# Performance work log

Hardware: AMD Instinct MI355X
Metric: run time of the kernel (lower is better)

The kernel has to match this reference:

```python
import jax, jax.numpy as jnp
import numpy as np

EPS = 1e-5  # BatchNorm eps (eval mode)
K_MAIN = 10
K_CORR = 8
LRELU = 0.2


def _knn_idx(x, k):
    # x: [B, c, n] -> [B, n, k] indices of k nearest neighbors (negative sq. distance top-k)
    inner = -2.0 * jnp.einsum('bcn,bcm->bnm', x, x)
    xx = jnp.sum(x * x, axis=1)                      # [B, n]
    pd = -xx[:, :, None] - inner - xx[:, None, :]    # [B, n, n]
    return jax.lax.top_k(pd, k)[1]


def _gather_neighbors(x, idx):
    # x: [B, c, n], idx: [B, n, k] -> [B, n, k, c]
    xt = jnp.transpose(x, (0, 2, 1))
    B = x.shape[0]
    return xt[jnp.arange(B)[:, None, None], idx]


def _graph_feature(x, k):
    # torch get_graph_feature: cat(neighbor - center, center) -> [B, 2c, n, k]
    idx = _knn_idx(x, k)
    neigh = _gather_neighbors(x, idx)                 # [B, n, k, c]
    xt = jnp.transpose(x, (0, 2, 1))                  # [B, n, c]
    center = jnp.broadcast_to(xt[:, :, None, :], neigh.shape)
    feat = jnp.concatenate([neigh - center, center], axis=-1)
    return jnp.transpose(feat, (0, 3, 1, 2))


def _branch(feat, w, g, b, m, v):
    # 1x1 Conv2d (no bias) + BatchNorm2d (eval) + LeakyReLU(0.2)
    y = jnp.einsum('oc,bcnk->bonk', w, feat)
    s = (g / jnp.sqrt(v + EPS))[None, :, None, None]
    y = (y - m[None, :, None, None]) * s + b[None, :, None, None]
    return jnp.where(y > 0, y, LRELU * y)


def _erase(x, masks, soft, w_e, b_e, g_e, be_e, m_e, v_e):
    # erase_feature: masked-softmax attention pooling + 1x1 conv_erase (conv+BN)
    soft = soft - (1.0 - masks) * 1e8
    sm = jax.nn.softmax(soft, axis=1)                 # [B, n]
    inp = x * masks[:, None, :]
    res = jnp.einsum('bcn,bn->bc', x, sm)             # [B, c]
    y = jnp.einsum('oc,bc->bo', w_e, res) + b_e
    y = (y - m_e) * (g_e / jnp.sqrt(v_e + EPS)) + be_e
    return inp + y[:, :, None]


def _corre_binar(x0_, x2, w_reduce):
    # x0_: [B, c] (detached query), x2: [B, c, n]
    B, c, n = x2.shape
    q = jnp.einsum('oc,bc->bo', w_reduce, x0_)        # conv_reduce (1x1, no bias)
    scale = 1.0 / jnp.sqrt(jnp.asarray(c, x2.dtype))
    f = jnp.einsum('bc,bcn->bn', q, x2) * scale       # [B, n]
    idx8 = _knn_idx(x2, K_CORR)                       # [B, n, 8]
    neigh = _gather_neighbors(x2, idx8)               # [B, n, 8, c]
    fk = jnp.einsum('bc,bnkc->bnk', q, neigh) * scale
    fk = f + jnp.sum(fk, axis=-1)                     # [B, n]
    index = jnp.argmax(fk, axis=1)                    # [B]
    ib = jnp.arange(B)
    masks = jnp.zeros((B, n), x2.dtype).at[ib, index].set(1.0)
    index_k = idx8[ib, index]                         # [B, 8] neighbors of argmax point
    masks = masks.at[ib[:, None], index_k].set(1.0)
    return 1.0 - masks, f


def _forward(x, w_reduce, w_erase, b_erase, g_erase, be_erase, m_erase, v_erase,
             w0, g0, b0, m0, v0, w1, g1, b1, m1, v1):
    b, t, c, n = x.shape
    B = b * t
    x1seq = jnp.concatenate([x[:, 1:], x[:, -1:]], axis=1).reshape(B, c, n)
    ones = jnp.ones((B, n), x.dtype)
    x0 = _erase(x.reshape(B, c, n), ones, ones,
                w_erase, b_erase, g_erase, be_erase, m_erase, v_erase)
    y0 = jnp.max(_branch(_graph_feature(x0, K_MAIN), w0, g0, b0, m0, v0), axis=-1)  # [B, O, n]
    x0_vec = jnp.max(y0, axis=-1)                                                    # [B, O]
    p0 = jnp.concatenate([jnp.max(y0, axis=-1), jnp.mean(y0, axis=-1)], axis=1)
    masks, soft = _corre_binar(jax.lax.stop_gradient(x0_vec), x1seq, w_reduce)
    x1e = _erase(x1seq, masks, soft,
                 w_erase, b_erase, g_erase, be_erase, m_erase, v_erase)
    y1 = jnp.max(_branch(_graph_feature(x1e, K_MAIN), w1, g1, b1, m1, v1), axis=-1)
    p1 = jnp.concatenate([jnp.max(y1, axis=-1), jnp.mean(y1, axis=-1)], axis=1)
    return p0 + p1                                                                   # [B, 2*O]


def setup_inputs() -> dict:
    key = jax.random.key(0)
    ks = jax.random.split(key, 20)
    b, t, c, n, out = 8, 12, 64, 512, 64
    sc = np.sqrt(2.0 / c).astype(np.float32)
    scb = np.sqrt(2.0 / out).astype(np.float32)
    f32 = jnp.float32
    inp = {
        'x': jax.random.normal(ks[0], (b, t, c, n), f32),
        'w_reduce': jax.random.normal(ks[1], (c, c), f32) * sc,
        'w_erase': jax.random.normal(ks[2], (c, c), f32) * sc,
        'b_erase': jax.random.normal(ks[3], (c,), f32) * 0.01,
        'g_erase': jax.random.uniform(ks[4], (c,), f32, 0.5, 1.5),
        'be_erase': jax.random.normal(ks[5], (c,), f32) * 0.1,
        'm_erase': jax.random.normal(ks[6], (c,), f32) * 0.1,
        'v_erase': jax.random.uniform(ks[7], (c,), f32, 0.5, 1.5),
        'w0': jax.random.normal(ks[8], (out, 2 * c), f32) * scb,
        'g0': jax.random.uniform(ks[9], (out,), f32, 0.5, 1.5),
        'b0': jax.random.normal(ks[10], (out,), f32) * 0.1,
        'm0': jax.random.normal(ks[11], (out,), f32) * 0.1,
        'v0': jax.random.uniform(ks[12], (out,), f32, 0.5, 1.5),
        'w1': jax.random.normal(ks[13], (out, 2 * c), f32) * scb,
        'g1': jax.random.uniform(ks[14], (out,), f32, 0.5, 1.5),
        'b1': jax.random.normal(ks[15], (out,), f32) * 0.1,
        'm1': jax.random.normal(ks[16], (out,), f32) * 0.1,
        'v1': jax.random.uniform(ks[17], (out,), f32, 0.5, 1.5),
    }
    return inp


def reference(x, w_reduce, w_erase, b_erase, g_erase, be_erase, m_erase, v_erase,
              w0, g0, b0, m0, v0, w1, g1, b1, m1, v1):
    return _forward(x, w_reduce, w_erase, b_erase, g_erase, be_erase, m_erase, v_erase,
                    w0, g0, b0, m0, v0, w1, g1, b1, m1, v1)
```

## Files before the change

kernel.cpp:

```cpp
#include <hip/hip_runtime.h>
#include <math.h>

#define EPS 1e-5f

typedef _Float16 half8 __attribute__((ext_vector_type(8)));
typedef float f32x4 __attribute__((ext_vector_type(4)));


__device__ __forceinline__ int src_row(int bq) {
    int b = bq / 12, t = bq - b * 12;
    int t2 = (t + 1 < 12) ? (t + 1) : 11;
    return b * 12 + t2;
}

__global__ __launch_bounds__(256) void prep_kernel(
    const float* __restrict__ X,
    _Float16* __restrict__ H, _Float16* __restrict__ L, float* __restrict__ xn,
    const float* __restrict__ w0, const float* __restrict__ w1,
    _Float16* __restrict__ wh0, _Float16* __restrict__ wl0,
    _Float16* __restrict__ wh1, _Float16* __restrict__ wl1,
    const float* __restrict__ w_e, const float* __restrict__ b_e,
    const float* __restrict__ g_e, const float* __restrict__ be_e,
    const float* __restrict__ m_e, const float* __restrict__ v_e,
    float* __restrict__ bias0)
{
    __shared__ float lds[64 * 65];
    __shared__ float xnp[4 * 64];
    __shared__ float part[256];
    __shared__ float res[64];
    __shared__ float sy[64];
    int raw = blockIdx.x;
    int tid = threadIdx.x;
    if (raw >= 768) {
        int bq = raw - 768;
        int c = tid >> 2, p = tid & 3;
        const float* xb = X + (size_t)bq * 32768 + c * 512 + p * 128;
        float acc = 0.f;
        for (int ii = 0; ii < 128; ii += 4) {
            float4 v = *(const float4*)(xb + ii);
            acc += v.x + v.y + v.z + v.w;
        }
        part[tid] = acc;
        __syncthreads();
        if (p == 0) res[c] = (part[tid] + part[tid+1] + part[tid+2] + part[tid+3]) * (1.f/512.f);
        __syncthreads();
        if (tid < 64) {
            float a = b_e[tid];
            for (int cc = 0; cc < 64; ++cc) a += w_e[tid*64+cc] * res[cc];
            float s = g_e[tid] / sqrtf(v_e[tid] + EPS);
            sy[tid] = (a - m_e[tid]) * s + be_e[tid];
        }
        __syncthreads();
        if (tid < 64) {
            float a = 0.f;
            for (int cc = 0; cc < 64; ++cc) a += w0[tid * 128 + 64 + cc] * sy[cc];
            bias0[bq * 64 + tid] = a;
        }
        return;
    }
    int bq = raw % 96;
    int ct = raw / 96;
    const float* Xb = X + (size_t)bq * 32768 + ct * 64;
    for (int p = 0; p < 16; ++p) {
        int t = p * 256 + tid;
        int c = t >> 6, col = t & 63;
        lds[c * 65 + col] = Xb[c * 512 + col];
    }
    __syncthreads();
    int col = tid & 63, g = tid >> 6;
    half8 hv[2], lv[2];
    float s = 0.f;
    #pragma unroll
    for (int k = 0; k < 16; ++k) {
        int c = g * 16 + k;
        float v = lds[c * 65 + col];
        _Float16 h = (_Float16)v;
        _Float16 lo = (_Float16)(v - (float)h);
        hv[k >> 3][k & 7] = h;
        lv[k >> 3][k & 7] = lo;
        s += v * v;
    }
    size_t obase = (size_t)bq * 32768 + ((size_t)(ct * 8 + 2 * g) * 64 + col) * 8;
    *(half8*)(H + obase) = hv[0];
    *(half8*)(H + obase + 512) = hv[1];
    *(half8*)(L + obase) = lv[0];
    *(half8*)(L + obase + 512) = lv[1];
    xnp[g * 64 + col] = s;
    __syncthreads();
    if (tid < 64)
        xn[bq * 512 + ct * 64 + tid] =
            xnp[tid] + xnp[64 + tid] + xnp[128 + tid] + xnp[192 + tid];
    if (raw < 2) {
        const float* W = raw ? w1 : w0;
        _Float16* WH = raw ? wh1 : wh0;
        _Float16* WL = raw ? wl1 : wl0;
        for (int t = tid; t < 8192; t += 256) {
            int o = t >> 6, c = t & 63;
            float v = (o < 64) ? W[o * 128 + c]
                               : (W[(o - 64) * 128 + 64 + c] - W[(o - 64) * 128 + c]);
            _Float16 h = (_Float16)v;
            WH[t] = h;
            WL[t] = (_Float16)(v - (float)h);
        }
    }
}

__global__ __launch_bounds__(256, 4) void knn_kernel(
    const _Float16* __restrict__ H, const _Float16* __restrict__ L,
    const float* __restrict__ xn,
    unsigned short* __restrict__ idx_out, unsigned short* __restrict__ key_out)
{
    __shared__ float4 jbuf[2048];
    int raw = blockIdx.x;
    int bq = raw % 96;
    int itile = raw / 96;
    int tid = threadIdx.x, w = tid >> 6, l = tid & 63;
    int lane16 = l & 15, quad = l >> 4;
    const size_t base = (size_t)bq * 32768;
    const _Float16* Hb = H + base;
    const _Float16* Lb = L + base;

    int irow = itile * 64 + w * 16 + lane16;
    size_t bo = ((size_t)(itile * 8 + quad) * 64 + (w * 16 + lane16)) * 8;
    half8 Bh0 = *(const half8*)(Hb + bo);
    half8 Bh1 = *(const half8*)(Hb + bo + 2048);
    half8 Bl0 = *(const half8*)(Lb + bo);
    half8 Bl1 = *(const half8*)(Lb + bo + 2048);

    unsigned kv[20];
    #pragma unroll
    for (int qq = 0; qq < 20; ++qq) kv[qq] = 0u;

    auto casu = [](unsigned& a, unsigned& b) {
        unsigned mn = a < b ? a : b;
        unsigned mx = a < b ? b : a;
        a = mn; b = mx;
    };

    const float* xnb = xn + bq * 512;
    float4* jbH = jbuf;
    float4* jbL = jbuf + 1024;
    {
        const float4* gh = (const float4*)(Hb);
        const float4* gl = (const float4*)(Lb);
        jbH[tid] = gh[tid]; jbH[256 + tid] = gh[256 + tid];
        jbL[tid] = gl[tid]; jbL[256 + tid] = gl[256 + tid];
    }
    __syncthreads();
    for (int jt = 0; jt < 8; ++jt) {
        int cur = jt & 1;
        float4 pa0, pa1, pb0, pb1;
        if (jt < 7) {
            const float4* gh = (const float4*)(Hb + (jt + 1) * 4096);
            const float4* gl = (const float4*)(Lb + (jt + 1) * 4096);
            pa0 = gh[tid]; pa1 = gh[256 + tid];
            pb0 = gl[tid]; pb1 = gl[256 + tid];
        }
        const _Float16* jH = (const _Float16*)(jbH + cur * 512);
        const _Float16* jL = (const _Float16*)(jbL + cur * 512);
        unsigned scb = (unsigned)((7 - jt) << 4);
        unsigned d[16];
        #pragma unroll
        for (int g = 0; g < 4; ++g) {
            int u = quad * 64 + g * 16 + lane16;
            half8 Ah0 = *(const half8*)(jH + (size_t)u * 8);
            half8 Ah1 = *(const half8*)(jH + (size_t)u * 8 + 2048);
            half8 Al0 = *(const half8*)(jL + (size_t)u * 8);
            half8 Al1 = *(const half8*)(jL + (size_t)u * 8 + 2048);
            f32x4 acc = {0.f, 0.f, 0.f, 0.f};
            acc = __builtin_amdgcn_mfma_f32_16x16x32_f16(Ah0, Bh0, acc, 0, 0, 0);
            acc = __builtin_amdgcn_mfma_f32_16x16x32_f16(Ah1, Bh1, acc, 0, 0, 0);
            acc = __builtin_amdgcn_mfma_f32_16x16x32_f16(Al0, Bh0, acc, 0, 0, 0);
            acc = __builtin_amdgcn_mfma_f32_16x16x32_f16(Al1, Bh1, acc, 0, 0, 0);
            acc = __builtin_amdgcn_mfma_f32_16x16x32_f16(Ah0, Bl0, acc, 0, 0, 0);
            acc = __builtin_amdgcn_mfma_f32_16x16x32_f16(Ah1, Bl1, acc, 0, 0, 0);
            int jb = jt * 64 + g * 16 + quad * 4;
            float4 xn4 = *(const float4*)&xnb[jb];
            #pragma unroll
            for (int r = 0; r < 4; ++r) {
                float xnr = (r == 0 ? xn4.x : r == 1 ? xn4.y : r == 2 ? xn4.z : xn4.w);
                float sc = fmaf(2.f, acc[r], -xnr);
                int bi = __float_as_int(sc);
                unsigned u2 = (unsigned)(bi ^ ((bi >> 31) | 0x80000000));
                int slot = g * 4 + r;
                d[slot] = (u2 & 0xFFFFFF80u) | (scb | (unsigned)(15 - slot));
            }
        }
        #pragma unroll
        for (int p = 1; p < 16; p <<= 1) {
            #pragma unroll
            for (int k = p; k >= 1; k >>= 1) {
                #pragma unroll
                for (int j = k & (p - 1); j + k < 16; j += 2 * k) {
                    #pragma unroll
                    for (int i = 0; i < k; ++i) {
                        if ((i + j + k < 16) &&
                            ((i + j) / (2 * p) == (i + j + k) / (2 * p)))
                            casu(d[i + j], d[i + j + k]);
                    }
                }
            }
        }
        #pragma unroll
        for (int i = 0; i < 16; ++i) {
            unsigned dv = d[15 - i];
            kv[i] = kv[i] > dv ? kv[i] : dv;
        }
        casu(kv[0],kv[16]); casu(kv[1],kv[17]); casu(kv[2],kv[18]); casu(kv[3],kv[19]);
        casu(kv[0],kv[8]);  casu(kv[1],kv[9]);  casu(kv[2],kv[10]); casu(kv[3],kv[11]);
        casu(kv[4],kv[12]); casu(kv[5],kv[13]); casu(kv[6],kv[14]); casu(kv[7],kv[15]);
        casu(kv[0],kv[4]);  casu(kv[1],kv[5]);  casu(kv[2],kv[6]);  casu(kv[3],kv[7]);
        casu(kv[8],kv[12]); casu(kv[9],kv[13]); casu(kv[10],kv[14]); casu(kv[11],kv[15]);
        casu(kv[0],kv[2]);  casu(kv[1],kv[3]);  casu(kv[4],kv[6]);  casu(kv[5],kv[7]);
        casu(kv[8],kv[10]); casu(kv[9],kv[11]); casu(kv[12],kv[14]); casu(kv[13],kv[15]);
        casu(kv[16],kv[18]); casu(kv[17],kv[19]);
        casu(kv[0],kv[1]);  casu(kv[2],kv[3]);  casu(kv[4],kv[5]);  casu(kv[6],kv[7]);
        casu(kv[8],kv[9]);  casu(kv[10],kv[11]); casu(kv[12],kv[13]); casu(kv[14],kv[15]);
        casu(kv[16],kv[17]); casu(kv[18],kv[19]);

        if (jt < 7) {
            jbH[(1 - cur) * 512 + tid] = pa0; jbH[(1 - cur) * 512 + 256 + tid] = pa1;
            jbL[(1 - cur) * 512 + tid] = pb0; jbL[(1 - cur) * 512 + 256 + tid] = pb1;
        }
        __syncthreads();
    }
    unsigned* MVb = (unsigned*)jbuf;
    #pragma unroll
    for (int qq = 0; qq < 20; ++qq)
        MVb[w * 1344 + (lane16 * 4 + quad) * 21 + qq] = kv[qq];
    __syncthreads();
    if (quad == 0) {
        const unsigned* MV = (const unsigned*)jbuf + w * 1344 + lane16 * 84;
        int p0 = 19, p1 = 19, p2 = 19, p3 = 19;
        unsigned short* op = idx_out + ((size_t)bq * 512 + irow) * 20;
        unsigned short* kp = key_out + ((size_t)bq * 512 + irow) * 20;
        for (int t = 0; t < 20; ++t) {
            unsigned bv = 0u; int bj = 0x7fffffff; int bc = -1;
            {   unsigned v = MV[p0];
                int bits = (int)(v & 127u), jtv = 7 - (bits >> 4), cod = 15 - (bits & 15);
                int j = jtv * 64 + ((cod >> 2) << 4) + (cod & 3);
                if (v > bv || (v == bv && j < bj)) { bv = v; bj = j; bc = 0; } }
            {   unsigned v = MV[21 + p1];
                int bits = (int)(v & 127u), jtv = 7 - (bits >> 4), cod = 15 - (bits & 15);
                int j = jtv * 64 + ((cod >> 2) << 4) + 4 + (cod & 3);
                if (v > bv || (v == bv && j < bj)) { bv = v; bj = j; bc = 1; } }
            {   unsigned v = MV[42 + p2];
                int bits = (int)(v & 127u), jtv = 7 - (bits >> 4), cod = 15 - (bits & 15);
                int j = jtv * 64 + ((cod >> 2) << 4) + 8 + (cod & 3);
                if (v > bv || (v == bv && j < bj)) { bv = v; bj = j; bc = 2; } }
            {   unsigned v = MV[63 + p3];
                int bits = (int)(v & 127u), jtv = 7 - (bits >> 4), cod = 15 - (bits & 15);
                int j = jtv * 64 + ((cod >> 2) << 4) + 12 + (cod & 3);
                if (v > bv || (v == bv && j < bj)) { bv = v; bj = j; bc = 3; } }
            if (bc == 0) --p0; else if (bc == 1) --p1; else if (bc == 2) --p2; else --p3;
            op[t] = (unsigned short)bj;
            kp[t] = (unsigned short)(bv >> 16);
        }
    }
}

__global__ __launch_bounds__(256) void derive_kernel(
    const float* __restrict__ x, const float* __restrict__ x0vec,
    const float* __restrict__ w_reduce,
    const unsigned short* __restrict__ idxA, const unsigned short* __restrict__ keyA,
    const float* __restrict__ xn,
    const float* __restrict__ w_e, const float* __restrict__ b_e,
    const float* __restrict__ g_e, const float* __restrict__ be_e,
    const float* __restrict__ m_e, const float* __restrict__ v_e,
    const float* __restrict__ w1,
    unsigned short* __restrict__ idxB, float* __restrict__ masks_out,
    float* __restrict__ bias1_out)
{
    __shared__ float ss[512];
    __shared__ float sw8[512];
    __shared__ float redf[256];
    __shared__ float sxv[64];
    __shared__ float sq[64];
    __shared__ float sres[64];
    __shared__ float syy[64];
    __shared__ float smask[512];
    __shared__ float xnl[512];
    __shared__ float redv[4];
    __shared__ int redi[4];
    __shared__ int mlist[12];
    __shared__ int mcnt;
    __shared__ int nmin[12];
    int bq = blockIdx.x;
    int row = src_row(bq);
    int tid = threadIdx.x, w = tid >> 6, l = tid & 63;
    const float* Xb = x + (size_t)row * 32768;

    if (tid < 64) sxv[tid] = x0vec[bq * 64 + tid];
    __syncthreads();
    if (tid < 64) {
        float a = 0.f;
        for (int c = 0; c < 64; ++c) a += w_reduce[tid * 64 + c] * sxv[c];
        sq[tid] = a;
    }
    __syncthreads();
    for (int i = tid; i < 512; i += 256) {
        float a = 0.f;
        for (int c = 0; c < 64; ++c) a += sq[c] * Xb[c * 512 + i];
        ss[i] = a * 0.125f;
    }
    __syncthreads();
    for (int i = tid; i < 512; i += 256) {
        float a = ss[i];
        const unsigned short* ip = idxA + ((size_t)row * 512 + i) * 20;
        for (int q = 0; q < 8; ++q) a += ss[ip[q]];
        sw8[i] = a;
        smask[i] = 1.0f;
    }
    __syncthreads();
    {
        float bv = sw8[tid]; int bi = tid;
        float v1 = sw8[tid + 256];
        if (v1 > bv) { bv = v1; bi = tid + 256; }
        #pragma unroll
        for (int off = 32; off >= 1; off >>= 1) {
            float ov = __shfl_down(bv, off);
            int oi = __shfl_down(bi, off);
            if (ov > bv || (ov == bv && oi < bi)) { bv = ov; bi = oi; }
        }
        if (l == 0) { redv[w] = bv; redi[w] = bi; }
    }
    __syncthreads();
    if (tid == 0) {
        float Bv = redv[0]; int Bi = redi[0];
        for (int ww = 1; ww < 4; ++ww)
            if (redv[ww] > Bv || (redv[ww] == Bv && redi[ww] < Bi)) { Bv = redv[ww]; Bi = redi[ww]; }
        smask[Bi] = 0.f;
        const unsigned short* ip = idxA + ((size_t)row * 512 + Bi) * 20;
        int c[9];
        c[0] = Bi;
        for (int q = 0; q < 8; ++q) { int j = ip[q]; smask[j] = 0.f; c[q + 1] = j; }
        for (int i2 = 1; i2 < 9; ++i2) {
            int v = c[i2]; int j2 = i2 - 1;
            while (j2 >= 0 && c[j2] > v) { c[j2 + 1] = c[j2]; --j2; }
            c[j2 + 1] = v;
        }
        int mc = 0, prev = -1;
        for (int i2 = 0; i2 < 9; ++i2)
            if (c[i2] != prev) { mlist[mc++] = c[i2]; prev = c[i2]; }
        mcnt = mc;
    }
    __syncthreads();
    masks_out[bq * 512 + tid] = smask[tid];
    masks_out[bq * 512 + tid + 256] = smask[tid + 256];
    int need = 10 - mcnt;
    float mk0 = smask[tid], mk1 = smask[tid + 256];
    float s0 = ss[tid] - (1.f - mk0) * 1e8f, s1 = ss[tid + 256] - (1.f - mk1) * 1e8f;
    redf[tid] = fmaxf(s0, s1);
    __syncthreads();
    for (int off = 128; off >= 1; off >>= 1) {
        if (tid < off) redf[tid] = fmaxf(redf[tid], redf[tid + off]);
        __syncthreads();
    }
    float mx = redf[0];
    __syncthreads();
    float e0 = expf(s0 - mx), e1 = expf(s1 - mx);
    redf[tid] = e0 + e1;
    __syncthreads();
    for (int off = 128; off >= 1; off >>= 1) {
        if (tid < off) redf[tid] = redf[tid] + redf[tid + off];
        __syncthreads();
    }
    float inv = 1.f / redf[0];
    __syncthreads();
    sw8[tid] = e0 * inv; sw8[tid + 256] = e1 * inv;
    xnl[tid] = xn[row * 512 + tid];
    xnl[tid + 256] = xn[row * 512 + tid + 256];
    __syncthreads();
    {
        int c4 = tid >> 2, p4 = tid & 3;
        float a = 0.f;
        const float* xr = Xb + c4 * 512 + p4 * 128;
        const float* wr = &sw8[p4 * 128];
        for (int ii = 0; ii < 128; ++ii) a += xr[ii] * wr[ii];
        redf[tid] = a;
    }
    __syncthreads();
    if ((tid & 3) == 0) {
        int c4 = tid >> 2;
        sres[c4] = redf[tid] + redf[tid + 1] + redf[tid + 2] + redf[tid + 3];
    }
    __syncthreads();
    if (tid < 64) {
        float a = b_e[tid];
        for (int cc = 0; cc < 64; ++cc) a += w_e[tid * 64 + cc] * sres[cc];
        float sc2 = g_e[tid] / sqrtf(v_e[tid] + EPS);
        syy[tid] = (a - m_e[tid]) * sc2 + be_e[tid];
    }
    __syncthreads();
    if (tid < 64) {
        float a = 0.f;
        for (int cc = 0; cc < 64; ++cc) a += w1[tid * 128 + 64 + cc] * syy[cc];
        bias1_out[bq * 64 + tid] = a;
    }
    for (int r = 0; r < need; ++r) {
        float bv; int bi;
        {
            float v0 = (smask[tid] != 0.f) ? xnl[tid] : 3.4e38f;
            float v1 = (smask[tid + 256] != 0.f) ? xnl[tid + 256] : 3.4e38f;
            bv = v0; bi = tid;
            if (v1 < bv) { bv = v1; bi = tid + 256; }
            #pragma unroll
            for (int off = 32; off >= 1; off >>= 1) {
                float ov = __shfl_down(bv, off);
                int oi = __shfl_down(bi, off);
                if (ov < bv || (ov == bv && oi < bi)) { bv = ov; bi = oi; }
            }
            if (l == 0) { redv[w] = bv; redi[w] = bi; }
        }
        __syncthreads();
        if (tid == 0) {
            float Bv = redv[0]; int Bi = redi[0];
            for (int ww = 1; ww < 4; ++ww)
                if (redv[ww] < Bv || (redv[ww] == Bv && redi[ww] < Bi)) { Bv = redv[ww]; Bi = redi[ww]; }
            nmin[r] = Bi;
            xnl[Bi] = 3.4e38f;
        }
        __syncthreads();
    }
    #pragma unroll
    for (int half = 0; half < 2; ++half) {
        int i = tid + half * 256;
        unsigned short* op = idxB + ((size_t)bq * 512 + i) * 10;
        if (smask[i] == 0.f) {
            int t2 = 0;
            for (int k = 0; k < mcnt; ++k) op[t2++] = (unsigned short)mlist[k];
            for (int r = 0; t2 < 10; ++r) op[t2++] = (unsigned short)nmin[r];
        } else {
            const unsigned short* ja = idxA + ((size_t)row * 512 + i) * 20;
            const unsigned short* ka = keyA + ((size_t)row * 512 + i) * 20;
            int pa = 0, pb = 0;
            for (int t2 = 0; t2 < 10; ++t2) {
                while (smask[ja[pa]] == 0.f) ++pa;
                unsigned kva = ka[pa];
                int jva = ja[pa];
                bool takeA = (pb >= mcnt) || (kva > 0x8000u) ||
                             (kva == 0x8000u && jva < mlist[pb]);
                if (takeA) { op[t2] = (unsigned short)jva; ++pa; }
                else       { op[t2] = (unsigned short)mlist[pb]; ++pb; }
            }
        }
    }
}

template<int ACC>
__global__ void __attribute__((amdgpu_flat_work_group_size(256, 256), amdgpu_waves_per_eu(2, 4)))
fused_branch_kernel(
    const _Float16* __restrict__ H, const _Float16* __restrict__ L,
    const _Float16* __restrict__ WH, const _Float16* __restrict__ WL,
    const unsigned short* __restrict__ idx, int istride,
    const float* __restrict__ masks, int remap,
    const float* __restrict__ bias,
    const float* __restrict__ g, const float* __restrict__ bb,
    const float* __restrict__ mm, const float* __restrict__ vv,
    float* __restrict__ out_p, float* __restrict__ vec_out)
{
    __shared__ float ldsA[8 * 512];
    __shared__ float ldsB[8 * 512];
    __shared__ unsigned short ldsIdx[512 * 10];
    __shared__ float smask[512];
    int bq = blockIdx.x, ob = blockIdx.y * 8;
    int row = remap ? src_row(bq) : bq;
    bool use_mask = (masks != nullptr);
    int tid = threadIdx.x, w = tid >> 6, l = tid & 63;
    int lane16 = l & 15, quad = l >> 4;
    const size_t base = (size_t)row * 32768;
    for (int p = 0; p < 20; ++p) {
        int t = p * 256 + tid;
        int i = t / 10, q = t - i * 10;
        ldsIdx[t] = idx[((size_t)bq * 512 + i) * istride + q];
    }
    if (use_mask) {
        smask[tid] = masks[bq * 512 + tid];
        smask[tid + 256] = masks[bq * 512 + tid + 256];
    }
    __syncthreads();
    {
        int wrow = (lane16 < 8) ? (ob + lane16) : (64 + ob + (lane16 - 8));
        size_t woff = (size_t)wrow * 64 + quad * 8;
        half8 Ah0 = *(const half8*)(WH + woff);
        half8 Ah1 = *(const half8*)(WH + woff + 32);
        half8 Al0 = *(const half8*)(WL + woff);
        half8 Al1 = *(const half8*)(WL + woff + 32);
        float* dst = (quad < 2) ? (ldsA + (quad * 4) * 512) : (ldsB + ((quad - 2) * 4) * 512);
        for (int k = 0; k < 8; ++k) {
            int it = w * 8 + k;
            size_t off = base + (((size_t)(it >> 2) * 8 + quad) * 64 + (it & 3) * 16 + lane16) * 8;
            half8 Xh0 = *(const half8*)(H + off);
            half8 Xh1 = *(const half8*)(H + off + 2048);
            half8 Xl0 = *(const half8*)(L + off);
            half8 Xl1 = *(const half8*)(L + off + 2048);
            if (use_mask) {
                float m = smask[it * 16 + lane16];
                if (m == 0.f) {
                    half8 z = {};
                    Xh0 = z; Xh1 = z; Xl0 = z; Xl1 = z;
                }
            }
            f32x4 acc = {0.f, 0.f, 0.f, 0.f};
            acc = __builtin_amdgcn_mfma_f32_16x16x32_f16(Ah0, Xh0, acc, 0, 0, 0);
            acc = __builtin_amdgcn_mfma_f32_16x16x32_f16(Ah1, Xh1, acc, 0, 0, 0);
            acc = __builtin_amdgcn_mfma_f32_16x16x32_f16(Ah0, Xl0, acc, 0, 0, 0);
            acc = __builtin_amdgcn_mfma_f32_16x16x32_f16(Ah1, Xl1, acc, 0, 0, 0);
            acc = __builtin_amdgcn_mfma_f32_16x16x32_f16(Al0, Xh0, acc, 0, 0, 0);
            acc = __builtin_amdgcn_mfma_f32_16x16x32_f16(Al1, Xh1, acc, 0, 0, 0);
            #pragma unroll
            for (int r = 0; r < 4; ++r)
                dst[r * 512 + it * 16 + lane16] = acc[r];
        }
    }
    __syncthreads();
    float ssr[2], str[2];
    #pragma unroll
    for (int oo = 0; oo < 2; ++oo) {
        int o = ob + w * 2 + oo;
        float sc = g[o] / sqrtf(vv[o] + EPS);
        ssr[oo] = sc;
        str[oo] = bb[o] - mm[o] * sc + bias[bq * 64 + o] * sc;
    }
    float omax[2], osum[2];
    #pragma unroll
    for (int oo = 0; oo < 2; ++oo) { omax[oo] = -3.4e38f; osum[oo] = 0.f; }
    const float* Aw = ldsA + (w * 2) * 512;
    const float* Bw = ldsB + (w * 2) * 512;
    for (int s = 0; s < 8; ++s) {
        int i = l + 64 * s;
        int idr[10];
        const unsigned short* ip = &ldsIdx[i * 10];
        #pragma unroll
        for (int q = 0; q < 10; ++q) idr[q] = ip[q];
        #pragma unroll
        for (int oo = 0; oo < 2; ++oo) {
            const float* Ao = Aw + oo * 512;
            float mx = Ao[idr[0]];
            #pragma unroll
            for (int q = 1; q < 10; ++q) mx = fmaxf(mx, Ao[idr[q]]);
            float val = (mx + Bw[oo * 512 + i]) * ssr[oo] + str[oo];
            float y = val > 0.f ? val : 0.2f * val;
            omax[oo] = fmaxf(omax[oo], y);
            osum[oo] += y;
        }
    }
    #pragma unroll
    for (int oo = 0; oo < 2; ++oo) {
        float M = omax[oo], S = osum[oo];
        #pragma unroll
        for (int off = 32; off >= 1; off >>= 1) {
            M = fmaxf(M, __shfl_down(M, off));
            S += __shfl_down(S, off);
        }
        if (l == 0) {
            int o = ob + w * 2 + oo;
            float* po = out_p + bq * 128;
            if (ACC) {
                po[o] += M;
                po[64 + o] += S * (1.f / 512.f);
            } else {
                po[o] = M;
                po[64 + o] = S * (1.f / 512.f);
                vec_out[bq * 64 + o] = M;
            }
        }
    }
}

extern "C" void kernel_launch(void* const* d_in, const int* in_sizes, int n_in,
                              void* d_out, int out_size, void* d_ws, size_t ws_size,
                              hipStream_t stream)
{
    const float* x        = (const float*)d_in[0];
    const float* w_reduce = (const float*)d_in[1];
    const float* w_erase  = (const float*)d_in[2];
    const float* b_erase  = (const float*)d_in[3];
    const float* g_erase  = (const float*)d_in[4];
    const float* be_erase = (const float*)d_in[5];
    const float* m_erase  = (const float*)d_in[6];
    const float* v_erase  = (const float*)d_in[7];
    const float* w0 = (const float*)d_in[8];
    const float* g0 = (const float*)d_in[9];
    const float* b0 = (const float*)d_in[10];
    const float* m0 = (const float*)d_in[11];
    const float* v0 = (const float*)d_in[12];
    const float* w1 = (const float*)d_in[13];
    const float* g1 = (const float*)d_in[14];
    const float* b1 = (const float*)d_in[15];
    const float* m1 = (const float*)d_in[16];
    const float* v1 = (const float*)d_in[17];
    float* out = (float*)d_out;
    char* ws = (char*)d_ws;

    _Float16* h0 = (_Float16*)(ws);
    _Float16* l0 = (_Float16*)(ws + 6291456);
    unsigned short* idxA = (unsigned short*)(ws + 12582912);
    unsigned short* keyA = (unsigned short*)(ws + 14548992);
    unsigned short* idxB = (unsigned short*)(ws + 16515072);
    float* xn0   = (float*)(ws + 17498112);
    float* bias0 = (float*)(ws + 17694720);
    float* bias1 = (float*)(ws + 17719296);
    float* x0vec = (float*)(ws + 17743872);
    float* masks = (float*)(ws + 17768448);
    _Float16* wh0 = (_Float16*)(ws + 17965056);
    _Float16* wl0 = (_Float16*)(ws + 17981440);
    _Float16* wh1 = (_Float16*)(ws + 17997824);
    _Float16* wl1 = (_Float16*)(ws + 18014208);

    (void)in_sizes; (void)n_in; (void)out_size; (void)ws_size;

    prep_kernel<<<864, 256, 0, stream>>>(x, h0, l0, xn0, w0, w1, wh0, wl0, wh1, wl1,
                                         w_erase, b_erase, g_erase, be_erase, m_erase, v_erase, bias0);
    knn_kernel<<<768, 256, 0, stream>>>(h0, l0, xn0, idxA, keyA);
    fused_branch_kernel<0><<<dim3(96, 8), 256, 0, stream>>>(h0, l0, wh0, wl0, idxA, 20,
                                                            nullptr, 0, bias0,
                                                            g0, b0, m0, v0, out, x0vec);
    derive_kernel<<<96, 256, 0, stream>>>(x, x0vec, w_reduce, idxA, keyA, xn0,
                                          w_erase, b_erase, g_erase, be_erase, m_erase, v_erase,
                                          w1, idxB, masks, bias1);
    fused_branch_kernel<1><<<dim3(96, 8), 256, 0, stream>>>(h0, l0, wh1, wl1, idxB, 10,
                                                            masks, 1, bias1,
                                                            g1, b1, m1, v1, out, nullptr);
}
```

Measured before the change: 214.1 us.

## Widen derive_kernel to 1024 threads with LDS-staged indices and shuffle reductions

The derive kernel runs on only 96 blocks, so it now uses 1024 threads per block instead of 256. Each small matvec (w_reduce, w_erase, w1) and the weighted pooling over x are split across 16 threads and finished with a partial-sum reduction. The per-row kNN index and key tables are copied into LDS with coalesced 32-bit loads, the softmax tree reductions become wave shuffles, and the idxB output is packed into 32-bit stores. These target the latency of a serial, under-occupied kernel on the critical path, at the cost of about 40KB of extra LDS and more barriers.

```diff
diff --git a/kernel.cpp b/kernel.cpp
--- a/kernel.cpp
+++ b/kernel.cpp
@@ -259,7 +259,7 @@
     }
 }
 
-__global__ __launch_bounds__(256) void derive_kernel(
+__global__ __launch_bounds__(1024) void derive_kernel(
     const float* __restrict__ x, const float* __restrict__ x0vec,
     const float* __restrict__ w_reduce,
     const unsigned short* __restrict__ idxA, const unsigned short* __restrict__ keyA,
@@ -271,66 +271,92 @@
     unsigned short* __restrict__ idxB, float* __restrict__ masks_out,
     float* __restrict__ bias1_out)
 {
+    __shared__ unsigned short sja[512 * 20];
+    __shared__ unsigned short ska[512 * 20];
     __shared__ float ss[512];
     __shared__ float sw8[512];
-    __shared__ float redf[256];
-    __shared__ float sxv[64];
-    __shared__ float sq[64];
-    __shared__ float sres[64];
-    __shared__ float syy[64];
     __shared__ float smask[512];
     __shared__ float xnl[512];
-    __shared__ float redv[4];
-    __shared__ int redi[4];
+    __shared__ float pl[1024];
+    __shared__ float sxv[64], sq[64], sres[64], syy[64];
+    __shared__ float redv[8];
+    __shared__ int   redi[8];
+    __shared__ float redf[8];
+    __shared__ float redf2[8];
     __shared__ int mlist[12];
-    __shared__ int mcnt;
     __shared__ int nmin[12];
+    __shared__ int s_mcnt, s_need;
+
     int bq = blockIdx.x;
     int row = src_row(bq);
-    int tid = threadIdx.x, w = tid >> 6, l = tid & 63;
+    int tid = threadIdx.x;
+    int w = tid >> 6, l = tid & 63;
     const float* Xb = x + (size_t)row * 32768;
 
+    {
+        const unsigned* gja = (const unsigned*)(idxA + (size_t)row * 10240);
+        const unsigned* gka = (const unsigned*)(keyA + (size_t)row * 10240);
+        unsigned* dja = (unsigned*)sja;
+        unsigned* dka = (unsigned*)ska;
+        #pragma unroll
+        for (int t = 0; t < 5; ++t) dja[t * 1024 + tid] = gja[t * 1024 + tid];
+        #pragma unroll
+        for (int t = 0; t < 5; ++t) dka[t * 1024 + tid] = gka[t * 1024 + tid];
+    }
+    if (tid < 512) { xnl[tid] = xn[row * 512 + tid]; smask[tid] = 1.0f; }
     if (tid < 64) sxv[tid] = x0vec[bq * 64 + tid];
+    __syncthreads();
+    {
+        int o = tid >> 4, c0 = (tid & 15) * 4;
+        const float* wr = w_reduce + o * 64 + c0;
+        pl[tid] = wr[0]*sxv[c0] + wr[1]*sxv[c0+1] + wr[2]*sxv[c0+2] + wr[3]*sxv[c0+3];
+    }
     __syncthreads();
     if (tid < 64) {
         float a = 0.f;
-        for (int c = 0; c < 64; ++c) a += w_reduce[tid * 64 + c] * sxv[c];
+        #pragma unroll
+        for (int s = 0; s < 16; ++s) a += pl[tid * 16 + s];
         sq[tid] = a;
     }
     __syncthreads();
-    for (int i = tid; i < 512; i += 256) {
+    {
+        int i = tid >> 1, h = tid & 1;
         float a = 0.f;
-        for (int c = 0; c < 64; ++c) a += sq[c] * Xb[c * 512 + i];
-        ss[i] = a * 0.125f;
-    }
-    __syncthreads();
-    for (int i = tid; i < 512; i += 256) {
-        float a = ss[i];
-        const unsigned short* ip = idxA + ((size_t)row * 512 + i) * 20;
+        #pragma unroll
+        for (int k = 0; k < 32; ++k) {
+            int c = h * 32 + k;
+            a += sq[c] * Xb[c * 512 + i];
+        }
+        a += __shfl_xor(a, 1);
+        if (h == 0) ss[i] = a * 0.125f;
+    }
+    __syncthreads();
+    if (tid < 512) {
+        float a = ss[tid];
+        const unsigned short* ip = &sja[tid * 20];
+        #pragma unroll
         for (int q = 0; q < 8; ++q) a += ss[ip[q]];
-        sw8[i] = a;
-        smask[i] = 1.0f;
-    }
-    __syncthreads();
-    {
-        float bv = sw8[tid]; int bi = tid;
-        float v1 = sw8[tid + 256];
-        if (v1 > bv) { bv = v1; bi = tid + 256; }
+        sw8[tid] = a;
+    }
+    __syncthreads();
+    {
+        float bv = -3.4e38f; int bi = 0x7fffffff;
+        if (tid < 512) { bv = sw8[tid]; bi = tid; }
         #pragma unroll
         for (int off = 32; off >= 1; off >>= 1) {
             float ov = __shfl_down(bv, off);
             int oi = __shfl_down(bi, off);
             if (ov > bv || (ov == bv && oi < bi)) { bv = ov; bi = oi; }
         }
-        if (l == 0) { redv[w] = bv; redi[w] = bi; }
+        if (l == 0 && w < 8) { redv[w] = bv; redi[w] = bi; }
     }
     __syncthreads();
     if (tid == 0) {
         float Bv = redv[0]; int Bi = redi[0];
-        for (int ww = 1; ww < 4; ++ww)
+        for (int ww = 1; ww < 8; ++ww)
             if (redv[ww] > Bv || (redv[ww] == Bv && redi[ww] < Bi)) { Bv = redv[ww]; Bi = redi[ww]; }
         smask[Bi] = 0.f;
-        const unsigned short* ip = idxA + ((size_t)row * 512 + Bi) * 20;
+        const unsigned short* ip = &sja[Bi * 20];
         int c[9];
         c[0] = Bi;
         for (int q = 0; q < 8; ++q) { int j = ip[q]; smask[j] = 0.f; c[q + 1] = j; }
@@ -342,108 +368,135 @@
         int mc = 0, prev = -1;
         for (int i2 = 0; i2 < 9; ++i2)
             if (c[i2] != prev) { mlist[mc++] = c[i2]; prev = c[i2]; }
-        mcnt = mc;
-    }
-    __syncthreads();
-    masks_out[bq * 512 + tid] = smask[tid];
-    masks_out[bq * 512 + tid + 256] = smask[tid + 256];
-    int need = 10 - mcnt;
-    float mk0 = smask[tid], mk1 = smask[tid + 256];
-    float s0 = ss[tid] - (1.f - mk0) * 1e8f, s1 = ss[tid + 256] - (1.f - mk1) * 1e8f;
-    redf[tid] = fmaxf(s0, s1);
-    __syncthreads();
-    for (int off = 128; off >= 1; off >>= 1) {
-        if (tid < off) redf[tid] = fmaxf(redf[tid], redf[tid + off]);
-        __syncthreads();
-    }
-    float mx = redf[0];
-    __syncthreads();
-    float e0 = expf(s0 - mx), e1 = expf(s1 - mx);
-    redf[tid] = e0 + e1;
-    __syncthreads();
-    for (int off = 128; off >= 1; off >>= 1) {
-        if (tid < off) redf[tid] = redf[tid] + redf[tid + off];
-        __syncthreads();
-    }
-    float inv = 1.f / redf[0];
-    __syncthreads();
-    sw8[tid] = e0 * inv; sw8[tid + 256] = e1 * inv;
-    xnl[tid] = xn[row * 512 + tid];
-    xnl[tid + 256] = xn[row * 512 + tid + 256];
-    __syncthreads();
-    {
-        int c4 = tid >> 2, p4 = tid & 3;
+        s_mcnt = mc;
+        s_need = 10 - mc;
+    }
+    __syncthreads();
+    int mcreg = s_mcnt, need = s_need;
+    float sval = -3.4e38f;
+    if (tid < 512) {
+        masks_out[bq * 512 + tid] = smask[tid];
+        sval = ss[tid] - (1.f - smask[tid]) * 1e8f;
+    }
+    {
+        float m = sval;
+        #pragma unroll
+        for (int off = 32; off >= 1; off >>= 1) m = fmaxf(m, __shfl_down(m, off));
+        if (l == 0 && w < 8) redf[w] = m;
+    }
+    __syncthreads();
+    float mx = fmaxf(fmaxf(fmaxf(redf[0], redf[1]), fmaxf(redf[2], redf[3])),
+                     fmaxf(fmaxf(redf[4], redf[5]), fmaxf(redf[6], redf[7])));
+    float ev = 0.f;
+    if (tid < 512) ev = expf(sval - mx);
+    {
+        float s = ev;
+        #pragma unroll
+        for (int off = 32; off >= 1; off >>= 1) s += __shfl_down(s, off);
+        if (l == 0 && w < 8) redf2[w] = s;
+    }
+    __syncthreads();
+    {
+        float sum = ((redf2[0] + redf2[1]) + (redf2[2] + redf2[3])) +
+                    ((redf2[4] + redf2[5]) + (redf2[6] + redf2[7]));
+        float inv = 1.f / sum;
+        if (tid < 512) sw8[tid] = ev * inv;
+    }
+    __syncthreads();
+    {
+        int c = tid >> 4, sub = tid & 15;
+        const float4* xr = (const float4*)(Xb + c * 512 + sub * 32);
+        const float4* wr = (const float4*)(&sw8[sub * 32]);
         float a = 0.f;
-        const float* xr = Xb + c4 * 512 + p4 * 128;
-        const float* wr = &sw8[p4 * 128];
-        for (int ii = 0; ii < 128; ++ii) a += xr[ii] * wr[ii];
-        redf[tid] = a;
-    }
-    __syncthreads();
-    if ((tid & 3) == 0) {
-        int c4 = tid >> 2;
-        sres[c4] = redf[tid] + redf[tid + 1] + redf[tid + 2] + redf[tid + 3];
+        #pragma unroll
+        for (int k = 0; k < 8; ++k) {
+            float4 xv = xr[k], wv = wr[k];
+            a += xv.x * wv.x + xv.y * wv.y + xv.z * wv.z + xv.w * wv.w;
+        }
+        pl[tid] = a;
+    }
+    __syncthreads();
+    if (tid < 64) {
+        float a = 0.f;
+        #pragma unroll
+        for (int s = 0; s < 16; ++s) a += pl[tid * 16 + s];
+        sres[tid] = a;
+    }
+    __syncthreads();
+    {
+        int o = tid >> 4, c0 = (tid & 15) * 4;
+        const float* wr = w_e + o * 64 + c0;
+        pl[tid] = wr[0]*sres[c0] + wr[1]*sres[c0+1] + wr[2]*sres[c0+2] + wr[3]*sres[c0+3];
     }
     __syncthreads();
     if (tid < 64) {
         float a = b_e[tid];
-        for (int cc = 0; cc < 64; ++cc) a += w_e[tid * 64 + cc] * sres[cc];
+        #pragma unroll
+        for (int s = 0; s < 16; ++s) a += pl[tid * 16 + s];
         float sc2 = g_e[tid] / sqrtf(v_e[tid] + EPS);
         syy[tid] = (a - m_e[tid]) * sc2 + be_e[tid];
     }
     __syncthreads();
+    {
+        int o = tid >> 4, c0 = (tid & 15) * 4;
+        const float* wr = w1 + o * 128 + 64 + c0;
+        pl[tid] = wr[0]*syy[c0] + wr[1]*syy[c0+1] + wr[2]*syy[c0+2] + wr[3]*syy[c0+3];
+    }
+    __syncthreads();
     if (tid < 64) {
         float a = 0.f;
-        for (int cc = 0; cc < 64; ++cc) a += w1[tid * 128 + 64 + cc] * syy[cc];
+        #pragma unroll
+        for (int s = 0; s < 16; ++s) a += pl[tid * 16 + s];
         bias1_out[bq * 64 + tid] = a;
     }
     for (int r = 0; r < need; ++r) {
-        float bv; int bi;
-        {
-            float v0 = (smask[tid] != 0.f) ? xnl[tid] : 3.4e38f;
-            float v1 = (smask[tid + 256] != 0.f) ? xnl[tid + 256] : 3.4e38f;
-            bv = v0; bi = tid;
-            if (v1 < bv) { bv = v1; bi = tid + 256; }
-            #pragma unroll
-            for (int off = 32; off >= 1; off >>= 1) {
-                float ov = __shfl_down(bv, off);
-                int oi = __shfl_down(bi, off);
-                if (ov < bv || (ov == bv && oi < bi)) { bv = ov; bi = oi; }
-            }
-            if (l == 0) { redv[w] = bv; redi[w] = bi; }
-        }
+        float bv = 3.4e38f; int bi = 0x7fffffff;
+        if (tid < 512) {
+            bv = (smask[tid] != 0.f) ? xnl[tid] : 3.4e38f;
+            bi = tid;
+        }
+        #pragma unroll
+        for (int off = 32; off >= 1; off >>= 1) {
+            float ov = __shfl_down(bv, off);
+            int oi = __shfl_down(bi, off);
+            if (ov < bv || (ov == bv && oi < bi)) { bv = ov; bi = oi; }
+        }
+        if (l == 0 && w < 8) { redv[w] = bv; redi[w] = bi; }
         __syncthreads();
         if (tid == 0) {
             float Bv = redv[0]; int Bi = redi[0];
-            for (int ww = 1; ww < 4; ++ww)
+            for (int ww = 1; ww < 8; ++ww)
                 if (redv[ww] < Bv || (redv[ww] == Bv && redi[ww] < Bi)) { Bv = redv[ww]; Bi = redi[ww]; }
             nmin[r] = Bi;
             xnl[Bi] = 3.4e38f;
         }
         __syncthreads();
     }
-    #pragma unroll
-    for (int half = 0; half < 2; ++half) {
-        int i = tid + half * 256;
-        unsigned short* op = idxB + ((size_t)bq * 512 + i) * 10;
+    if (tid < 512) {
+        int i = tid;
+        unsigned short tmp[10];
         if (smask[i] == 0.f) {
             int t2 = 0;
-            for (int k = 0; k < mcnt; ++k) op[t2++] = (unsigned short)mlist[k];
-            for (int r = 0; t2 < 10; ++r) op[t2++] = (unsigned short)nmin[r];
+            for (int k2 = 0; k2 < mcreg; ++k2) tmp[t2++] = (unsigned short)mlist[k2];
+            for (int r = 0; t2 < 10; ++r) tmp[t2++] = (unsigned short)nmin[r];
         } else {
-            const unsigned short* ja = idxA + ((size_t)row * 512 + i) * 20;
-            const unsigned short* ka = keyA + ((size_t)row * 512 + i) * 20;
+            const unsigned short* ja = &sja[i * 20];
+            const unsigned short* ka = &ska[i * 20];
             int pa = 0, pb = 0;
             for (int t2 = 0; t2 < 10; ++t2) {
                 while (smask[ja[pa]] == 0.f) ++pa;
                 unsigned kva = ka[pa];
                 int jva = ja[pa];
-                bool takeA = (pb >= mcnt) || (kva > 0x8000u) ||
+                bool takeA = (pb >= mcreg) || (kva > 0x8000u) ||
                              (kva == 0x8000u && jva < mlist[pb]);
-                if (takeA) { op[t2] = (unsigned short)jva; ++pa; }
-                else       { op[t2] = (unsigned short)mlist[pb]; ++pb; }
+                if (takeA) { tmp[t2] = (unsigned short)jva; ++pa; }
+                else       { tmp[t2] = (unsigned short)mlist[pb]; ++pb; }
             }
         }
+        unsigned* op = (unsigned*)(idxB + (size_t)bq * 5120 + (size_t)i * 10);
+        #pragma unroll
+        for (int k2 = 0; k2 < 5; ++k2)
+            op[k2] = (unsigned)tmp[2 * k2] | ((unsigned)tmp[2 * k2 + 1] << 16);
     }
 }
 
@@ -616,9 +669,9 @@
     fused_branch_kernel<0><<<dim3(96, 8), 256, 0, stream>>>(h0, l0, wh0, wl0, idxA, 20,
                                                             nullptr, 0, bias0,
                                                             g0, b0, m0, v0, out, x0vec);
-    derive_kernel<<<96, 256, 0, stream>>>(x, x0vec, w_reduce, idxA, keyA, xn0,
-                                          w_erase, b_erase, g_erase, be_erase, m_erase, v_erase,
-                                          w1, idxB, masks, bias1);
+    derive_kernel<<<96, 1024, 0, stream>>>(x, x0vec, w_reduce, idxA, keyA, xn0,
+                                           w_erase, b_erase, g_erase, be_erase, m_erase, v_erase,
+                                           w1, idxB, masks, bias1);
     fused_branch_kernel<1><<<dim3(96, 8), 256, 0, stream>>>(h0, l0, wh1, wl1, idxB, 10,
                                                             masks, 1, bias1,
                                                             g1, b1, m1, v1, out, nullptr);
```

Result: faster. 186.6 us (-12.9%).
